# Kernel optimization log

Hardware: AMD Instinct MI355X
Metric: run time of the kernel (lower is better)

Reference implementation:

```python
import jax, jax.numpy as jnp
import numpy as np

E, K, N, T, TOPK, GROUP_SIZE = 8, 2048, 2048, 1024, 2, 128


def setup_inputs() -> dict:
    key = jax.random.key(0)
    ks = jax.random.split(key, 6)
    x = jax.random.normal(ks[0], (T, K), dtype=jnp.float32)
    # uint8-quantized weights stored as int32 (values 0..255)
    w_q = jax.random.randint(ks[1], (E, K, N), 0, 256, dtype=jnp.int32)
    scales = jax.random.uniform(ks[2], (E, K, K // GROUP_SIZE), dtype=jnp.float32) * 0.02
    zeros = jax.random.normal(ks[3], (E, K, K // GROUP_SIZE), dtype=jnp.float32) * 0.1
    topk_weights = jax.random.uniform(ks[4], (T, TOPK), dtype=jnp.float32)
    topk_ids = jax.random.randint(ks[5], (T, TOPK), 0, E, dtype=jnp.int32)
    return {"x": x, "w_q": w_q, "scales": scales, "zeros": zeros,
            "topk_weights": topk_weights, "topk_ids": topk_ids}


def reference(x, w_q, scales, zeros, topk_weights, topk_ids):
    # Faithful to _moe_kernel_w8a16: for each (token, expert-slot) pair,
    #   out[t, n] += topk_weight * sum_k x[t, k] * (w_q[e, k, n] * scales[e, k, k//gs] + zeros[e, k, k//gs])
    # Note the kernel broadcasts scale/zero over n (offs_n * 0) with group index k // group_size.
    k_idx = jnp.arange(K)
    g_idx = k_idx // GROUP_SIZE                      # (K,)
    s = scales[:, k_idx, g_idx]                       # (E, K) scale per (e, k)
    z = zeros[:, k_idx, g_idx]                        # (E, K)
    w_deq = w_q.astype(jnp.float32) * s[:, :, None] + z[:, :, None]  # (E, K, N)
    # dense per-expert GEMM, then gather the top_k experts per token
    all_out = jnp.einsum('tk,ekn->ten', x, w_deq)     # (T, E, N)
    sel = jnp.take_along_axis(all_out, topk_ids[:, :, None].astype(jnp.int32), axis=1)  # (T, TOPK, N)
    out = jnp.sum(sel * topk_weights[:, :, None], axis=1)  # (T, N)
    return out
```

## Files before the change

kernel.cpp:

```cpp
#include <hip/hip_runtime.h>
#include <hip/hip_bf16.h>
#include <stdint.h>

#define E_    8
#define K_    2048
#define N_    2048
#define T_    1024
#define TOPK_ 2
#define NG_   16
#define MAXM  512

#define BM 128
#define BN 64
#define BK 64
#define NST (K_ / BK)
#define MTILES (MAXM / BM)

typedef __attribute__((ext_vector_type(8))) short bf16x8;
typedef __attribute__((ext_vector_type(4))) float f32x4;
typedef __attribute__((ext_vector_type(4))) int i32x4;
typedef __attribute__((ext_vector_type(4))) unsigned int u32x4;
typedef __attribute__((ext_vector_type(8))) unsigned short u16x8;

__device__ __forceinline__ unsigned short f2bf_rne(float f) {
    unsigned u = __float_as_uint(f);
    u += 0x7fffu + ((u >> 16) & 1u);
    return (unsigned short)(u >> 16);
}
__device__ __forceinline__ unsigned short f2bf_trunc(float f) {
    return (unsigned short)(__float_as_uint(f) >> 16);
}

__global__ void prep_sz(const float* __restrict__ scales, const float* __restrict__ zeros,
                        float* __restrict__ sd, float* __restrict__ zd, int* __restrict__ cnt)
{
    int i = blockIdx.x * 256 + threadIdx.x;
    int e = i >> 11;
    int k = i & (K_ - 1);
    int g = k >> 7;
    size_t src = ((size_t)e * K_ + k) * NG_ + g;
    sd[i] = scales[src];
    zd[i] = zeros[src];
    if (i < E_) cnt[i] = 0;
}

__global__ void route_k(const int* __restrict__ topk_ids, int* __restrict__ cnt,
                        int* __restrict__ ptj)
{
    int idx = blockIdx.x * 256 + threadIdx.x;
    if (idx < T_ * TOPK_) {
        int e = topk_ids[idx];
        int slot = atomicAdd(&cnt[e], 1);
        if (slot < T_ * TOPK_) ptj[e * (T_ * TOPK_) + slot] = idx;
    }
}

__global__ void zdot_k(const float* __restrict__ x, const float* __restrict__ zdiag,
                       const int* __restrict__ topk_ids, float* __restrict__ zdot)
{
    int w = (int)((blockIdx.x * blockDim.x + threadIdx.x) >> 6);
    int lane = threadIdx.x & 63;
    int t = w >> 1;
    int e = topk_ids[w];
    const f32x4* xp = (const f32x4*)(x + (size_t)t * K_);
    const f32x4* zp = (const f32x4*)(zdiag + (size_t)e * K_);
    float acc = 0.f;
#pragma unroll
    for (int it = 0; it < K_ / 256; ++it) {
        f32x4 a = xp[it * 64 + lane];
        f32x4 b = zp[it * 64 + lane];
        acc += a.x * b.x + a.y * b.y + a.z * b.z + a.w * b.w;
    }
#pragma unroll
    for (int off = 32; off > 0; off >>= 1) acc += __shfl_xor(acc, off);
    if (lane == 0) zdot[w] = acc;
}

__global__ void aprep_k(const float* __restrict__ x, const float* __restrict__ sdiag,
                        const int* __restrict__ cnt, const int* __restrict__ ptj,
                        unsigned short* __restrict__ apack)
{
    int e = blockIdx.y;
    int slot = blockIdx.x;
    if (slot >= min(cnt[e], MAXM)) return;
    int tj = ptj[e * (T_ * TOPK_) + slot];
    int t = tj >> 1;
    const float* xr = x + (size_t)t * K_;
    const float* sr = sdiag + (size_t)e * K_;
    int k = threadIdx.x * 8;
    f32x4 a0 = *(const f32x4*)(xr + k);
    f32x4 s0 = *(const f32x4*)(sr + k);
    f32x4 a1 = *(const f32x4*)(xr + k + 4);
    f32x4 s1 = *(const f32x4*)(sr + k + 4);
    u16x8 h;
    h[0] = f2bf_rne(a0.x * s0.x);
    h[1] = f2bf_rne(a0.y * s0.y);
    h[2] = f2bf_rne(a0.z * s0.z);
    h[3] = f2bf_rne(a0.w * s0.w);
    h[4] = f2bf_rne(a1.x * s1.x);
    h[5] = f2bf_rne(a1.y * s1.y);
    h[6] = f2bf_rne(a1.z * s1.z);
    h[7] = f2bf_rne(a1.w * s1.w);
    *(u16x8*)(apack + ((size_t)e * MAXM + slot) * K_ + k) = h;
}

__global__ __launch_bounds__(256, 3)
void moe_gemm(const int* __restrict__ wq, const unsigned short* __restrict__ apack,
              const float* __restrict__ topk_w, const int* __restrict__ cnt,
              const int* __restrict__ ptj, const float* __restrict__ zdot,
              float* __restrict__ part, float* __restrict__ out, int use_part)
{
    int e = blockIdx.z;
    int count = min(cnt[e], MAXM);
    int m0 = blockIdx.y * BM;
    if (m0 >= count) return;
    int n0 = blockIdx.x * BN;

    __shared__ alignas(16) unsigned short As[2][BM * BK];
    __shared__ alignas(16) unsigned short Bs[2][BN * BK];

    int tid = threadIdx.x;
    int lane = tid & 63;
    int wid = tid >> 6;
    int wm = (wid >> 1) * 64;
    int wn = (wid & 1) * 32;

    int arow = tid >> 3;
    int asl = tid & 7;
    const char* ag = (const char*)(apack + (size_t)e * MAXM * K_)
                   + ((size_t)(m0 + arow) * K_) * 2 + asl * 16;
    int alds = arow * 128 + ((asl ^ (arow & 7)) << 4);

    int b_n = tid & 63;
    int b_set = tid >> 6;
    const int* wcol = wq + (size_t)e * K_ * N_ + n0 + b_n;
    int bswz = (b_n & 7) << 4;

    f32x4 acc[4][2] = {};
    i32x4 a0[4], a1[4];
    int b0[16], b1[16], b2[16];

    auto loadA = [&](i32x4* dst, int kt) {
        const char* base = ag + (size_t)kt * (BK * 2);
#pragma unroll
        for (int r = 0; r < 4; ++r)
            dst[r] = *(const i32x4*)(base + (size_t)r * 32 * K_ * 2);
    };
    auto writeA = [&](const i32x4* src, int abuf) {
        char* l = (char*)As[abuf] + alds;
#pragma unroll
        for (int r = 0; r < 4; ++r)
            *(u32x4*)(l + r * 4096) = __builtin_bit_cast(u32x4, src[r]);
    };
    auto loadB = [&](int* br, int kt) {
        int kb = kt * BK + b_set * 16;
#pragma unroll
        for (int i = 0; i < 16; ++i)
            br[i] = wcol[(kb + i) * N_];
    };
    auto packB = [&](const int* br, int bbuf) {
        unsigned pk[8];
#pragma unroll
        for (int i = 0; i < 8; ++i) {
            unsigned lo = f2bf_trunc((float)br[2 * i]);
            unsigned hi = f2bf_trunc((float)br[2 * i + 1]);
            pk[i] = lo | (hi << 16);
        }
        char* bsrow = (char*)Bs[bbuf] + b_n * (BK * 2);
#pragma unroll
        for (int seg = 0; seg < 2; ++seg) {
            int kbyte = b_set * 32 + seg * 16;
            u32x4 v = { pk[seg * 4], pk[seg * 4 + 1], pk[seg * 4 + 2], pk[seg * 4 + 3] };
            *(u32x4*)(bsrow + (kbyte ^ bswz)) = v;
        }
    };
    auto comp = [&](int buf) {
#pragma unroll
        for (int kk2 = 0; kk2 < 2; ++kk2) {
            int kb = kk2 * 64 + ((lane >> 4) << 4);
            bf16x8 af[4], bfr[2];
#pragma unroll
            for (int mi = 0; mi < 4; ++mi) {
                int row = wm + mi * 16 + (lane & 15);
                af[mi] = *(const bf16x8*)((const char*)As[buf] + row * 128 + (kb ^ ((row & 7) << 4)));
            }
#pragma unroll
            for (int ni = 0; ni < 2; ++ni) {
                int row = wn + ni * 16 + (lane & 15);
                bfr[ni] = *(const bf16x8*)((const char*)Bs[buf] + row * 128 + (kb ^ ((row & 7) << 4)));
            }
#pragma unroll
            for (int mi = 0; mi < 4; ++mi)
#pragma unroll
                for (int ni = 0; ni < 2; ++ni)
                    acc[mi][ni] = __builtin_amdgcn_mfma_f32_16x16x32_bf16(
                        af[mi], bfr[ni], acc[mi][ni], 0, 0, 0);
        }
    };

    loadA(a0, 0);
    loadA(a1, 1);
    loadB(b0, 0);
    loadB(b1, 1);
    loadB(b2, 2);
    writeA(a0, 0);
    packB(b0, 0);
    asm volatile("s_waitcnt lgkmcnt(0)" ::: "memory");
    __builtin_amdgcn_s_barrier();
    asm volatile("" ::: "memory");

    int kt = 0;
#define STEP(AL, BL, CC, AW, BP) do {                                         \
        loadA(AL, kt + 2);                                                    \
        loadB(BL, min(kt + 3, NST - 1));                                      \
        comp(CC);                                                             \
        writeA(AW, CC ^ 1);                                                   \
        packB(BP, CC ^ 1);                                                    \
        asm volatile("s_waitcnt lgkmcnt(0)" ::: "memory");                    \
        __builtin_amdgcn_s_barrier();                                         \
        asm volatile("" ::: "memory");                                        \
        ++kt;                                                                 \
    } while (0)

#pragma unroll 1
    for (int it = 0; it < 5; ++it) {
        STEP(a0, b0, 0, a1, b1);
        STEP(a1, b1, 1, a0, b2);
        STEP(a0, b2, 0, a1, b0);
        STEP(a1, b0, 1, a0, b1);
        STEP(a0, b1, 0, a1, b2);
        STEP(a1, b2, 1, a0, b0);
    }
#undef STEP
    comp(0);
    writeA(a1, 1);
    packB(b1, 1);
    asm volatile("s_waitcnt lgkmcnt(0)" ::: "memory");
    __builtin_amdgcn_s_barrier();
    asm volatile("" ::: "memory");
    comp(1);

#pragma unroll
    for (int mi = 0; mi < 4; ++mi) {
        int prow = m0 + wm + mi * 16 + ((lane >> 4) << 2);
#pragma unroll
        for (int r = 0; r < 4; ++r) {
            int p = prow + r;
            if (p < count) {
                int tj = ptj[e * (T_ * TOPK_) + p];
                float w = topk_w[tj];
                float zdv = zdot[tj];
                float v0 = w * (acc[mi][0][r] + zdv);
                float v1 = w * (acc[mi][1][r] + zdv);
                if (use_part) {
                    float* pr = part + (size_t)tj * N_ + n0 + wn + (lane & 15);
                    pr[0]  = v0;
                    pr[16] = v1;
                } else {
                    float* orow = out + (size_t)(tj >> 1) * N_ + n0 + wn + (lane & 15);
                    atomicAdd(orow + 0,  v0);
                    atomicAdd(orow + 16, v1);
                }
            }
        }
    }
}

__global__ void reduce_k(const float* __restrict__ part, float* __restrict__ out)
{
    int g = blockIdx.x * 256 + threadIdx.x;
    int t = g >> 9;
    int nc = g & 511;
    f32x4 a = ((const f32x4*)part)[((size_t)(t * 2) << 9) + nc];
    f32x4 b = ((const f32x4*)part)[((size_t)(t * 2 + 1) << 9) + nc];
    ((f32x4*)out)[g] = a + b;
}

extern "C" void kernel_launch(void* const* d_in, const int* in_sizes, int n_in,
                              void* d_out, int out_size, void* d_ws, size_t ws_size,
                              hipStream_t stream)
{
    const float* x       = (const float*)d_in[0];
    const int*   wq      = (const int*)d_in[1];
    const float* scales  = (const float*)d_in[2];
    const float* zeros   = (const float*)d_in[3];
    const float* topk_w  = (const float*)d_in[4];
    const int*   topk_id = (const int*)d_in[5];
    float* out = (float*)d_out;

    char* ws = (char*)d_ws;
    float* sdiag = (float*)(ws + 0);
    float* zdiag = (float*)(ws + 65536);
    int*   cnt   = (int*)(ws + 131072);
    int*   ptj   = (int*)(ws + 135168);
    float* zdot  = (float*)(ws + 200704);
    unsigned short* apack = (unsigned short*)(ws + (1 << 20));
    float* part  = (float*)(ws + ((size_t)17 << 20));
    size_t need = ((size_t)17 << 20) + (size_t)T_ * TOPK_ * N_ * sizeof(float);
    int use_part = (ws_size >= need) ? 1 : 0;

    prep_sz<<<E_ * K_ / 256, 256, 0, stream>>>(scales, zeros, sdiag, zdiag, cnt);
    route_k<<<T_ * TOPK_ / 256, 256, 0, stream>>>(topk_id, cnt, ptj);
    zdot_k<<<T_ * TOPK_ / 4, 256, 0, stream>>>(x, zdiag, topk_id, zdot);
    aprep_k<<<dim3(MAXM, E_), 256, 0, stream>>>(x, sdiag, cnt, ptj, apack);
    if (!use_part)
        hipMemsetAsync(d_out, 0, (size_t)T_ * N_ * sizeof(float), stream);
    moe_gemm<<<dim3(N_ / BN, MTILES, E_), 256, 0, stream>>>(
        wq, apack, topk_w, cnt, ptj, zdot, part, out, use_part);
    if (use_part)
        reduce_k<<<T_ * N_ / 4 / 256, 256, 0, stream>>>(part, out);
}
```

Baseline: 90.14 us.

## Load weight tiles row-wise with 16-byte vectors and store K-major in LDS

Weight loading changes from per-thread column reads of 16 scalar ints strided by N to coalesced 16-byte vector loads along N. The tile is stored in LDS K-major with a padded stride, and the fp32-to-bf16 packing is simplified. The cost is that the MFMA B fragment is now built from eight separate 16-bit LDS reads plus shift/or packing per fragment instead of one 128-bit read, which adds LDS instructions and possible bank conflicts in the inner loop.

Result: slower. 105.2 us (+16.7%).

```diff
diff --git a/kernel.cpp b/kernel.cpp
--- a/kernel.cpp
+++ b/kernel.cpp
@@ -15,10 +15,12 @@
 #define BK 64
 #define NST (K_ / BK)
 #define MTILES (MAXM / BM)
+#define BSTRIDE 68
 
 typedef __attribute__((ext_vector_type(8))) short bf16x8;
 typedef __attribute__((ext_vector_type(4))) float f32x4;
 typedef __attribute__((ext_vector_type(4))) int i32x4;
+typedef __attribute__((ext_vector_type(2))) unsigned int u32x2;
 typedef __attribute__((ext_vector_type(4))) unsigned int u32x4;
 typedef __attribute__((ext_vector_type(8))) unsigned short u16x8;
 
@@ -27,8 +29,9 @@
     u += 0x7fffu + ((u >> 16) & 1u);
     return (unsigned short)(u >> 16);
 }
-__device__ __forceinline__ unsigned short f2bf_trunc(float f) {
-    return (unsigned short)(__float_as_uint(f) >> 16);
+__device__ __forceinline__ unsigned pack2bf(int lo, int hi) {
+    float fl = (float)lo, fh = (float)hi;
+    return (__float_as_uint(fl) >> 16) | (__float_as_uint(fh) & 0xffff0000u);
 }
 
 __global__ void prep_sz(const float* __restrict__ scales, const float* __restrict__ zeros,
@@ -117,7 +120,7 @@
     int n0 = blockIdx.x * BN;
 
     __shared__ alignas(16) unsigned short As[2][BM * BK];
-    __shared__ alignas(16) unsigned short Bs[2][BN * BK];
+    __shared__ alignas(16) unsigned short Bs[2][BK * BSTRIDE];
 
     int tid = threadIdx.x;
     int lane = tid & 63;
@@ -131,14 +134,13 @@
                    + ((size_t)(m0 + arow) * K_) * 2 + asl * 16;
     int alds = arow * 128 + ((asl ^ (arow & 7)) << 4);
 
-    int b_n = tid & 63;
-    int b_set = tid >> 6;
-    const int* wcol = wq + (size_t)e * K_ * N_ + n0 + b_n;
-    int bswz = (b_n & 7) << 4;
+    int b_k = tid >> 2;
+    int b_ns = (tid & 3) * 4;
+    const int* brow = wq + (size_t)e * K_ * N_ + (size_t)b_k * N_ + n0 + b_ns;
 
     f32x4 acc[4][2] = {};
     i32x4 a0[4], a1[4];
-    int b0[16], b1[16], b2[16];
+    i32x4 b0[4], b1[4], b2[4];
 
     auto loadA = [&](i32x4* dst, int kt) {
         const char* base = ag + (size_t)kt * (BK * 2);
@@ -152,42 +154,42 @@
         for (int r = 0; r < 4; ++r)
             *(u32x4*)(l + r * 4096) = __builtin_bit_cast(u32x4, src[r]);
     };
-    auto loadB = [&](int* br, int kt) {
-        int kb = kt * BK + b_set * 16;
-#pragma unroll
-        for (int i = 0; i < 16; ++i)
-            br[i] = wcol[(kb + i) * N_];
-    };
-    auto packB = [&](const int* br, int bbuf) {
-        unsigned pk[8];
-#pragma unroll
-        for (int i = 0; i < 8; ++i) {
-            unsigned lo = f2bf_trunc((float)br[2 * i]);
-            unsigned hi = f2bf_trunc((float)br[2 * i + 1]);
-            pk[i] = lo | (hi << 16);
+    auto loadB = [&](i32x4* br, int kt) {
+        const int* src = brow + (size_t)kt * BK * N_;
+#pragma unroll
+        for (int i = 0; i < 4; ++i)
+            br[i] = *(const i32x4*)(src + i * 16);
+    };
+    auto writeB = [&](const i32x4* br, int bbuf) {
+        unsigned short* rowp = &Bs[bbuf][b_k * BSTRIDE];
+#pragma unroll
+        for (int i = 0; i < 4; ++i) {
+            i32x4 v = br[i];
+            u32x2 h = { pack2bf(v.x, v.y), pack2bf(v.z, v.w) };
+            *(u32x2*)(rowp + b_ns + i * 16) = h;
         }
-        char* bsrow = (char*)Bs[bbuf] + b_n * (BK * 2);
-#pragma unroll
-        for (int seg = 0; seg < 2; ++seg) {
-            int kbyte = b_set * 32 + seg * 16;
-            u32x4 v = { pk[seg * 4], pk[seg * 4 + 1], pk[seg * 4 + 2], pk[seg * 4 + 3] };
-            *(u32x4*)(bsrow + (kbyte ^ bswz)) = v;
-        }
     };
     auto comp = [&](int buf) {
 #pragma unroll
         for (int kk2 = 0; kk2 < 2; ++kk2) {
-            int kb = kk2 * 64 + ((lane >> 4) << 4);
+            int kbyte = kk2 * 64 + ((lane >> 4) << 4);
+            int kb = kk2 * 32 + ((lane >> 4) << 3);
             bf16x8 af[4], bfr[2];
 #pragma unroll
             for (int mi = 0; mi < 4; ++mi) {
                 int row = wm + mi * 16 + (lane & 15);
-                af[mi] = *(const bf16x8*)((const char*)As[buf] + row * 128 + (kb ^ ((row & 7) << 4)));
+                af[mi] = *(const bf16x8*)((const char*)As[buf] + row * 128 + (kbyte ^ ((row & 7) << 4)));
             }
 #pragma unroll
             for (int ni = 0; ni < 2; ++ni) {
-                int row = wn + ni * 16 + (lane & 15);
-                bfr[ni] = *(const bf16x8*)((const char*)Bs[buf] + row * 128 + (kb ^ ((row & 7) << 4)));
+                int ncol = wn + ni * 16 + (lane & 15);
+                const unsigned short* bp = &Bs[buf][kb * BSTRIDE + ncol];
+                unsigned d0 = (unsigned)bp[0]           | ((unsigned)bp[BSTRIDE]     << 16);
+                unsigned d1 = (unsigned)bp[2 * BSTRIDE] | ((unsigned)bp[3 * BSTRIDE] << 16);
+                unsigned d2 = (unsigned)bp[4 * BSTRIDE] | ((unsigned)bp[5 * BSTRIDE] << 16);
+                unsigned d3 = (unsigned)bp[6 * BSTRIDE] | ((unsigned)bp[7 * BSTRIDE] << 16);
+                union { unsigned u[4]; bf16x8 v; } f = {{ d0, d1, d2, d3 }};
+                bfr[ni] = f.v;
             }
 #pragma unroll
             for (int mi = 0; mi < 4; ++mi)
@@ -204,7 +206,7 @@
     loadB(b1, 1);
     loadB(b2, 2);
     writeA(a0, 0);
-    packB(b0, 0);
+    writeB(b0, 0);
     asm volatile("s_waitcnt lgkmcnt(0)" ::: "memory");
     __builtin_amdgcn_s_barrier();
     asm volatile("" ::: "memory");
@@ -215,7 +217,7 @@
         loadB(BL, min(kt + 3, NST - 1));                                      \
         comp(CC);                                                             \
         writeA(AW, CC ^ 1);                                                   \
-        packB(BP, CC ^ 1);                                                    \
+        writeB(BP, CC ^ 1);                                                   \
         asm volatile("s_waitcnt lgkmcnt(0)" ::: "memory");                    \
         __builtin_amdgcn_s_barrier();                                         \
         asm volatile("" ::: "memory");                                        \
@@ -234,7 +236,7 @@
 #undef STEP
     comp(0);
     writeA(a1, 1);
-    packB(b1, 1);
+    writeB(b1, 1);
     asm volatile("s_waitcnt lgkmcnt(0)" ::: "memory");
     __builtin_amdgcn_s_barrier();
     asm volatile("" ::: "memory");
```

## Pre-convert int32 weights to k-interleaved bf16 layout before GEMM

Applied to the files above, without the earlier changes.

Adds a bprep kernel that converts the int32 uint8 weights once per call into bf16 stored in a k-grouped-by-8, n-major layout. The GEMM then loads B with two 16-byte vector loads per thread instead of sixteen strided scalar int32 loads plus in-loop conversion. This removes the uncoalesced strided weight reads and the conversion ALU work from the GEMM's inner loop. In exchange it adds an extra pass that reads 128MB of int32 and writes 64MB of bf16, and it only runs when the workspace is large enough.

Result: slower. 105.5 us (+17.1%).

```diff
diff --git a/kernel.cpp b/kernel.cpp
--- a/kernel.cpp
+++ b/kernel.cpp
@@ -19,6 +19,7 @@
 typedef __attribute__((ext_vector_type(8))) short bf16x8;
 typedef __attribute__((ext_vector_type(4))) float f32x4;
 typedef __attribute__((ext_vector_type(4))) int i32x4;
+typedef __attribute__((ext_vector_type(2))) unsigned int u32x2;
 typedef __attribute__((ext_vector_type(4))) unsigned int u32x4;
 typedef __attribute__((ext_vector_type(8))) unsigned short u16x8;
 
@@ -27,8 +28,9 @@
     u += 0x7fffu + ((u >> 16) & 1u);
     return (unsigned short)(u >> 16);
 }
-__device__ __forceinline__ unsigned short f2bf_trunc(float f) {
-    return (unsigned short)(__float_as_uint(f) >> 16);
+__device__ __forceinline__ unsigned pack2bf(int lo, int hi) {
+    float fl = (float)lo, fh = (float)hi;
+    return (__float_as_uint(fl) >> 16) | (__float_as_uint(fh) & 0xffff0000u);
 }
 
 __global__ void prep_sz(const float* __restrict__ scales, const float* __restrict__ zeros,
@@ -104,8 +106,41 @@
     *(u16x8*)(apack + ((size_t)e * MAXM + slot) * K_ + k) = h;
 }
 
+__global__ void bprep_k(const int* __restrict__ wq, unsigned short* __restrict__ btp)
+{
+    int e = blockIdx.y;
+    int kb = blockIdx.x;
+    __shared__ unsigned short L[8][N_];
+    int tid = threadIdx.x;
+    const int* src = wq + ((size_t)e * K_ + (size_t)kb * 8) * N_;
+#pragma unroll
+    for (int i = 0; i < 16; ++i) {
+        i32x4 v = *(const i32x4*)(src + i * 1024 + tid * 4);
+        int k = i >> 1;
+        int n = (i & 1) * 1024 + tid * 4;
+        u32x2 h = { pack2bf(v.x, v.y), pack2bf(v.z, v.w) };
+        *(u32x2*)&L[k][n] = h;
+    }
+    __syncthreads();
+    unsigned short* dst = btp + (size_t)(e * 256 + kb) * (N_ * 8);
+#pragma unroll
+    for (int j = 0; j < 8; ++j) {
+        int n = j * 256 + tid;
+        unsigned d0 = (unsigned)L[0][n] | ((unsigned)L[1][n] << 16);
+        unsigned d1 = (unsigned)L[2][n] | ((unsigned)L[3][n] << 16);
+        unsigned d2 = (unsigned)L[4][n] | ((unsigned)L[5][n] << 16);
+        unsigned d3 = (unsigned)L[6][n] | ((unsigned)L[7][n] << 16);
+        u32x4 o = { d0, d1, d2, d3 };
+        *(u32x4*)(dst + (size_t)n * 8) = o;
+    }
+}
+
+struct BRegs { i32x4 v[2]; int l[16]; };
+
+template<int USE_BTP>
 __global__ __launch_bounds__(256, 3)
-void moe_gemm(const int* __restrict__ wq, const unsigned short* __restrict__ apack,
+void moe_gemm(const int* __restrict__ wq, const unsigned short* __restrict__ btp,
+              const unsigned short* __restrict__ apack,
               const float* __restrict__ topk_w, const int* __restrict__ cnt,
               const int* __restrict__ ptj, const float* __restrict__ zdot,
               float* __restrict__ part, float* __restrict__ out, int use_part)
@@ -132,13 +167,15 @@
     int alds = arow * 128 + ((asl ^ (arow & 7)) << 4);
 
     int b_n = tid & 63;
-    int b_set = tid >> 6;
+    int b_kq = tid >> 6;
+    int bswz = (b_n & 7) << 4;
+    const char* btb = (const char*)btp
+                    + ((size_t)e * 256 * N_ + (size_t)(n0 + b_n)) * 8 * 2;
     const int* wcol = wq + (size_t)e * K_ * N_ + n0 + b_n;
-    int bswz = (b_n & 7) << 4;
 
     f32x4 acc[4][2] = {};
     i32x4 a0[4], a1[4];
-    int b0[16], b1[16], b2[16];
+    BRegs b0, b1, b2;
 
     auto loadA = [&](i32x4* dst, int kt) {
         const char* base = ag + (size_t)kt * (BK * 2);
@@ -152,26 +189,35 @@
         for (int r = 0; r < 4; ++r)
             *(u32x4*)(l + r * 4096) = __builtin_bit_cast(u32x4, src[r]);
     };
-    auto loadB = [&](int* br, int kt) {
-        int kb = kt * BK + b_set * 16;
-#pragma unroll
-        for (int i = 0; i < 16; ++i)
-            br[i] = wcol[(kb + i) * N_];
-    };
-    auto packB = [&](const int* br, int bbuf) {
-        unsigned pk[8];
-#pragma unroll
-        for (int i = 0; i < 8; ++i) {
-            unsigned lo = f2bf_trunc((float)br[2 * i]);
-            unsigned hi = f2bf_trunc((float)br[2 * i + 1]);
-            pk[i] = lo | (hi << 16);
+    auto loadB = [&](BRegs& br, int kt) {
+        if constexpr (USE_BTP) {
+            const char* base = btb + (size_t)(kt * 8 + b_kq * 2) * 32768;
+            br.v[0] = *(const i32x4*)base;
+            br.v[1] = *(const i32x4*)(base + 32768);
+        } else {
+            int kb = kt * BK + b_kq * 16;
+#pragma unroll
+            for (int i = 0; i < 16; ++i)
+                br.l[i] = wcol[(kb + i) * N_];
         }
+    };
+    auto writeB = [&](const BRegs& br, int bbuf) {
         char* bsrow = (char*)Bs[bbuf] + b_n * (BK * 2);
-#pragma unroll
-        for (int seg = 0; seg < 2; ++seg) {
-            int kbyte = b_set * 32 + seg * 16;
-            u32x4 v = { pk[seg * 4], pk[seg * 4 + 1], pk[seg * 4 + 2], pk[seg * 4 + 3] };
-            *(u32x4*)(bsrow + (kbyte ^ bswz)) = v;
+        if constexpr (USE_BTP) {
+            int k0b = b_kq * 32;
+            *(u32x4*)(bsrow + (k0b ^ bswz)) = __builtin_bit_cast(u32x4, br.v[0]);
+            *(u32x4*)(bsrow + ((k0b + 16) ^ bswz)) = __builtin_bit_cast(u32x4, br.v[1]);
+        } else {
+            unsigned pk[8];
+#pragma unroll
+            for (int i = 0; i < 8; ++i)
+                pk[i] = pack2bf(br.l[2 * i], br.l[2 * i + 1]);
+#pragma unroll
+            for (int seg = 0; seg < 2; ++seg) {
+                int kbyte = b_kq * 32 + seg * 16;
+                u32x4 v = { pk[seg * 4], pk[seg * 4 + 1], pk[seg * 4 + 2], pk[seg * 4 + 3] };
+                *(u32x4*)(bsrow + (kbyte ^ bswz)) = v;
+            }
         }
     };
     auto comp = [&](int buf) {
@@ -204,7 +250,7 @@
     loadB(b1, 1);
     loadB(b2, 2);
     writeA(a0, 0);
-    packB(b0, 0);
+    writeB(b0, 0);
     asm volatile("s_waitcnt lgkmcnt(0)" ::: "memory");
     __builtin_amdgcn_s_barrier();
     asm volatile("" ::: "memory");
@@ -215,7 +261,7 @@
         loadB(BL, min(kt + 3, NST - 1));                                      \
         comp(CC);                                                             \
         writeA(AW, CC ^ 1);                                                   \
-        packB(BP, CC ^ 1);                                                    \
+        writeB(BP, CC ^ 1);                                                   \
         asm volatile("s_waitcnt lgkmcnt(0)" ::: "memory");                    \
         __builtin_amdgcn_s_barrier();                                         \
         asm volatile("" ::: "memory");                                        \
@@ -234,7 +280,7 @@
 #undef STEP
     comp(0);
     writeA(a1, 1);
-    packB(b1, 1);
+    writeB(b1, 1);
     asm volatile("s_waitcnt lgkmcnt(0)" ::: "memory");
     __builtin_amdgcn_s_barrier();
     asm volatile("" ::: "memory");
@@ -296,8 +342,11 @@
     float* zdot  = (float*)(ws + 200704);
     unsigned short* apack = (unsigned short*)(ws + (1 << 20));
     float* part  = (float*)(ws + ((size_t)17 << 20));
-    size_t need = ((size_t)17 << 20) + (size_t)T_ * TOPK_ * N_ * sizeof(float);
-    int use_part = (ws_size >= need) ? 1 : 0;
+    unsigned short* btp = (unsigned short*)(ws + ((size_t)34 << 20));
+    size_t need_part = ((size_t)17 << 20) + (size_t)T_ * TOPK_ * N_ * sizeof(float);
+    size_t need_btp  = ((size_t)34 << 20) + (size_t)E_ * K_ * N_ * 2;
+    int use_part = (ws_size >= need_part) ? 1 : 0;
+    int use_btp  = (ws_size >= need_btp) ? 1 : 0;
 
     prep_sz<<<E_ * K_ / 256, 256, 0, stream>>>(scales, zeros, sdiag, zdiag, cnt);
     route_k<<<T_ * TOPK_ / 256, 256, 0, stream>>>(topk_id, cnt, ptj);
@@ -305,8 +354,14 @@
     aprep_k<<<dim3(MAXM, E_), 256, 0, stream>>>(x, sdiag, cnt, ptj, apack);
     if (!use_part)
         hipMemsetAsync(d_out, 0, (size_t)T_ * N_ * sizeof(float), stream);
-    moe_gemm<<<dim3(N_ / BN, MTILES, E_), 256, 0, stream>>>(
-        wq, apack, topk_w, cnt, ptj, zdot, part, out, use_part);
+    if (use_btp) {
+        bprep_k<<<dim3(K_ / 8, E_), 256, 0, stream>>>(wq, btp);
+        moe_gemm<1><<<dim3(N_ / BN, MTILES, E_), 256, 0, stream>>>(
+            wq, btp, apack, topk_w, cnt, ptj, zdot, part, out, use_part);
+    } else {
+        moe_gemm<0><<<dim3(N_ / BN, MTILES, E_), 256, 0, stream>>>(
+            wq, btp, apack, topk_w, cnt, ptj, zdot, part, out, use_part);
+    }
     if (use_part)
         reduce_k<<<T_ * N_ / 4 / 256, 256, 0, stream>>>(part, out);
 }
```
